# Kernel optimization log

Hardware: AMD Instinct MI355X
Metric: run time of the kernel (lower is better)

The kernel has to match this reference:

```python
import jax, jax.numpy as jnp
import numpy as np
from jax import lax

N, DIM, K, B = 400000, 128, 27, 8


def setup_inputs() -> dict:
    key = jax.random.key(0)
    ks = jax.random.split(key, 8)
    feats = jax.random.normal(ks[0], (N, DIM), dtype=jnp.float32)
    neighbor_idx = jax.random.randint(ks[1], (N, K), 0, N, dtype=jnp.int32)
    neighbor_mask = jax.random.randint(ks[2], (N, K), 0, 2) > 0
    segment_ids = jnp.sort(jax.random.randint(ks[3], (N,), 0, B, dtype=jnp.int32))
    s = 1.0 / np.sqrt(DIM)
    W1 = jax.random.normal(ks[4], (K, DIM, DIM), dtype=jnp.float32) * s
    W2 = jax.random.normal(ks[5], (K, DIM, DIM), dtype=jnp.float32) * s
    W3 = jax.random.normal(ks[6], (DIM, DIM), dtype=jnp.float32) * s
    b1 = jnp.zeros((DIM,), jnp.float32)
    b2 = jnp.zeros((DIM,), jnp.float32)
    b3 = jnp.zeros((DIM,), jnp.float32)
    return {"feats": feats, "neighbor_idx": neighbor_idx, "neighbor_mask": neighbor_mask,
            "segment_ids": segment_ids, "num_segments": B,
            "W1": W1, "b1": b1, "W2": W2, "b2": b2, "W3": W3, "b3": b3}


def sparse_conv3(x, idx, mask, W, b):
    # x: [N,D]; idx/mask: [N,K]; W: [K,D,D] -> y[n] = sum_k mask[n,k] * x[idx[n,k]] @ W[k] + b
    def step(acc, kin):
        ik, mk, Wk = kin  # [N], [N], [D,D]
        g = jnp.where(mk[:, None], x[ik], 0.0)  # [N,D] gather per offset
        return acc + g @ Wk, None
    acc, _ = lax.scan(step, jnp.zeros_like(x), (idx.T, mask.T, W))
    return acc + b


def reference(feats, neighbor_idx, neighbor_mask, segment_ids, num_segments,
              W1, b1, W2, b2, W3, b3):
    out1 = jax.nn.relu(sparse_conv3(feats, neighbor_idx, neighbor_mask, W1, b1))
    out2 = jax.nn.relu(sparse_conv3(feats, neighbor_idx, neighbor_mask, W2, b2))
    # per-batch: outer(mean over channels of out1 [Ni,1], mean over points of out2 [1,D])
    sums = jax.ops.segment_sum(out2, segment_ids, num_segments=num_segments)  # [B,D]
    cnts = jax.ops.segment_sum(jnp.ones((out2.shape[0],), out2.dtype), segment_ids,
                               num_segments=num_segments)  # [B]
    seg_mean2 = sums / jnp.maximum(cnts, 1.0)[:, None]  # [B,D]
    row_mean1 = jnp.mean(out1, axis=-1, keepdims=True)  # [N,1]
    enc = jnp.sqrt(row_mean1 * seg_mean2[segment_ids] + 1e-12)  # [N,D]
    mid = enc + out1 + out2
    out3 = jax.nn.relu(mid @ W3 + b3)  # kernel_size=1 conv == pointwise linear
    return jax.nn.relu(feats - out3)
```

## Files before the change

### kernel.cpp

```cpp
#include <hip/hip_runtime.h>
#include <stdint.h>

#define NPTS 400000
#define DIM  128
#define KNB  27
#define NSEG 8

typedef _Float16 f16x8 __attribute__((ext_vector_type(8)));
typedef float floatx16 __attribute__((ext_vector_type(16)));

#define OFF_FEATSH 0UL
#define OFF_OUT1   102400000UL
#define OFF_OUT2   204800000UL
#define OFF_PW1    307200000UL
#define OFF_PW2    308084736UL
#define OFF_PW3    308969472UL
#define OFF_SEG    309002240UL
#define OFF_CNT    309006336UL

__device__ __forceinline__ void load_lds16(const void* g, void* l) {
  __builtin_amdgcn_global_load_lds(
      (const __attribute__((address_space(1))) void*)g,
      (__attribute__((address_space(3))) void*)l, 16, 0, 0);
}

__global__ __launch_bounds__(256) void cvt_feats(const float* __restrict__ f,
                                                 _Float16* __restrict__ fh) {
  size_t g = (size_t)blockIdx.x * 256 + threadIdx.x;
  const float4* src = (const float4*)f;
  float4 v0 = src[g * 2], v1 = src[g * 2 + 1];
  f16x8 o;
  o[0] = (_Float16)v0.x; o[1] = (_Float16)v0.y; o[2] = (_Float16)v0.z; o[3] = (_Float16)v0.w;
  o[4] = (_Float16)v1.x; o[5] = (_Float16)v1.y; o[6] = (_Float16)v1.z; o[7] = (_Float16)v1.w;
  ((f16x8*)fh)[g] = o;
}

__global__ __launch_bounds__(256) void pack_w(const float* __restrict__ W1,
                                              const float* __restrict__ W2,
                                              const float* __restrict__ W3,
                                              _Float16* __restrict__ pW1,
                                              _Float16* __restrict__ pW2,
                                              _Float16* __restrict__ pW3) {
  int gid = blockIdx.x * 256 + threadIdx.x;
  const float* W; _Float16* dst; int k, rem;
  if (gid < 110592) {
    int mat = gid / 55296, r = gid % 55296;
    W = mat ? W2 : W1; dst = (mat ? pW2 : pW1) + (size_t)r * 8;
    k = r >> 11; rem = r & 2047;
  } else {
    int r = gid - 110592;
    W = W3; dst = pW3 + (size_t)r * 8; k = 0; rem = r;
  }
  int ko = rem >> 8, ct = (rem >> 6) & 3, lane = rem & 63;
  int h = lane >> 5, c = ct * 32 + (lane & 31);
  f16x8 o;
#pragma unroll
  for (int j = 0; j < 8; ++j) {
    int kk = ko * 16 + h * 8 + j;
    o[j] = (_Float16)W[(size_t)(k * 128 + kk) * 128 + c];
  }
  *(f16x8*)dst = o;
}

__global__ __launch_bounds__(256, 2) void conv_kernel(
    const _Float16* __restrict__ featsh, const int* __restrict__ nidx,
    const int* __restrict__ nmask, const int* __restrict__ segids,
    const _Float16* __restrict__ pW1, const _Float16* __restrict__ pW2,
    const float* __restrict__ b1, const float* __restrict__ b2,
    _Float16* __restrict__ out1, _Float16* __restrict__ out2,
    float* __restrict__ seg_sums, float* __restrict__ cnts_f) {
  __shared__ __align__(16) char lds_raw[65536];
  int tid = threadIdx.x, w = tid >> 6, lane = tid & 63;
  int conv = w >> 1, g = w & 1, h = lane >> 5;
  int n0 = blockIdx.x * 128;
  int row0 = n0 + g * 64 + (lane & 31);
  int row1 = row0 + 32;

  floatx16 acc0[4], acc1[4];
#pragma unroll
  for (int ct = 0; ct < 4; ++ct)
#pragma unroll
    for (int r = 0; r < 16; ++r) { acc0[ct][r] = 0.f; acc1[ct][r] = 0.f; }

  const char* srcW = (const char*)(w < 2 ? pW1 : pW2) + (w & 1) * 16384;

  for (int k = 0; k < KNB; ++k) {
    __syncthreads();
    const char* sk = srcW + (size_t)k * 32768;
    char* ldsb = lds_raw + w * 16384;
#pragma unroll
    for (int it = 0; it < 16; ++it)
      load_lds16(sk + it * 1024 + lane * 16, ldsb + it * 1024);
    int i0 = nidx[row0 * KNB + k]; int m0 = nmask[row0 * KNB + k];
    int i1 = nidx[row1 * KNB + k]; int m1 = nmask[row1 * KNB + k];
    __syncthreads();
    const _Float16* ldsW = (const _Float16*)(lds_raw + conv * 32768);
    const _Float16* ar0 = featsh + (size_t)i0 * 128 + h * 8;
    const _Float16* ar1 = featsh + (size_t)i1 * 128 + h * 8;
#pragma unroll
    for (int ko = 0; ko < 8; ++ko) {
      uint4 a0u = {0, 0, 0, 0}, a1u = {0, 0, 0, 0};
      if (m0) a0u = *(const uint4*)(ar0 + ko * 16);
      if (m1) a1u = *(const uint4*)(ar1 + ko * 16);
      f16x8 a0 = __builtin_bit_cast(f16x8, a0u);
      f16x8 a1 = __builtin_bit_cast(f16x8, a1u);
#pragma unroll
      for (int ct = 0; ct < 4; ++ct) {
        f16x8 b = *(const f16x8*)(ldsW + ((ko * 4 + ct) * 64 + lane) * 8);
        acc0[ct] = __builtin_amdgcn_mfma_f32_32x32x16_f16(a0, b, acc0[ct], 0, 0, 0);
        acc1[ct] = __builtin_amdgcn_mfma_f32_32x32x16_f16(a1, b, acc1[ct], 0, 0, 0);
      }
    }
  }

  const float* bb = conv ? b2 : b1;
  float bias[4];
#pragma unroll
  for (int ct = 0; ct < 4; ++ct) bias[ct] = bb[ct * 32 + (lane & 31)];
#pragma unroll
  for (int ct = 0; ct < 4; ++ct)
#pragma unroll
    for (int r = 0; r < 16; ++r) {
      acc0[ct][r] = fmaxf(acc0[ct][r] + bias[ct], 0.f);
      acc1[ct][r] = fmaxf(acc1[ct][r] + bias[ct], 0.f);
    }

  int seg0 = segids[n0];
  bool uniform = (seg0 == segids[n0 + 127]);

  if (conv == 1 && uniform) {
#pragma unroll
    for (int ct = 0; ct < 4; ++ct) {
      float s = 0.f;
#pragma unroll
      for (int r = 0; r < 16; ++r) s += acc0[ct][r] + acc1[ct][r];
      s += __shfl_xor(s, 32);
      if (lane < 32) atomicAdd(&seg_sums[seg0 * 128 + ct * 32 + lane], s);
    }
  }
  if (tid == 0 && uniform) atomicAdd(&cnts_f[seg0], 128.0f);

  __syncthreads();
  _Float16* lds_out = (_Float16*)lds_raw;
#pragma unroll
  for (int ct = 0; ct < 4; ++ct) {
    int col = ct * 32 + (lane & 31);
#pragma unroll
    for (int r = 0; r < 16; ++r) {
      int lr = g * 64 + (r & 3) + 8 * (r >> 2) + 4 * h;
      lds_out[conv * 16384 + lr * 128 + col] = (_Float16)acc0[ct][r];
      lds_out[conv * 16384 + (lr + 32) * 128 + col] = (_Float16)acc1[ct][r];
    }
  }
  __syncthreads();

  if (!uniform && tid < 128) {
    int s = segids[n0 + tid];
    atomicAdd(&cnts_f[s], 1.0f);
    for (int c = 0; c < 128; ++c)
      atomicAdd(&seg_sums[s * 128 + c], (float)lds_out[16384 + tid * 128 + c]);
  }

#pragma unroll
  for (int it = 0; it < 16; ++it) {
    int chunk = it * 256 + tid;
    int cv = chunk >> 11;
    int off16 = chunk & 2047;
    uint4 v = *(const uint4*)(lds_raw + cv * 32768 + off16 * 16);
    *(uint4*)((cv ? out2 : out1) + (size_t)n0 * 128 + off16 * 8) = v;
  }
}

__global__ __launch_bounds__(256, 2) void final_kernel(
    const float* __restrict__ feats, const _Float16* __restrict__ out1,
    const _Float16* __restrict__ out2, const int* __restrict__ segids,
    const float* __restrict__ seg_sums, const float* __restrict__ cnts_f,
    const char* __restrict__ pW3, const float* __restrict__ b3,
    float* __restrict__ dout) {
  __shared__ __align__(16) char ldsw3[32768];
  __shared__ float smean[NSEG * 128];
  int tid = threadIdx.x, w = tid >> 6, lane = tid & 63, h = lane >> 5;
  int n0 = blockIdx.x * 128;
#pragma unroll
  for (int it = 0; it < 8; ++it)
    load_lds16(pW3 + w * 8192 + it * 1024 + lane * 16, ldsw3 + w * 8192 + it * 1024);
  for (int i = tid; i < NSEG * 128; i += 256)
    smean[i] = seg_sums[i] / fmaxf(cnts_f[i >> 7], 1.0f);
  __syncthreads();

  int row = n0 + w * 32 + (lane & 31);
  int seg = segids[row];
  const char* p1 = (const char*)(out1 + (size_t)row * 128 + h * 8);
  const char* p2 = (const char*)(out2 + (size_t)row * 128 + h * 8);
  f16x8 o1[8], o2[8];
  float s1 = 0.f;
#pragma unroll
  for (int ko = 0; ko < 8; ++ko) {
    o1[ko] = *(const f16x8*)(p1 + ko * 32);
    o2[ko] = *(const f16x8*)(p2 + ko * 32);
#pragma unroll
    for (int j = 0; j < 8; ++j) s1 += (float)o1[ko][j];
  }
  s1 += __shfl_xor(s1, 32);
  float rm = s1 * (1.0f / 128.0f);

  f16x8 a[8];
#pragma unroll
  for (int ko = 0; ko < 8; ++ko) {
    int colb = ko * 16 + h * 8;
#pragma unroll
    for (int j = 0; j < 8; ++j) {
      float m2 = smean[seg * 128 + colb + j];
      float e = sqrtf(fmaf(rm, m2, 1e-12f));
      a[ko][j] = (_Float16)(e + (float)o1[ko][j] + (float)o2[ko][j]);
    }
  }
  floatx16 acc[4];
#pragma unroll
  for (int ct = 0; ct < 4; ++ct)
#pragma unroll
    for (int r = 0; r < 16; ++r) acc[ct][r] = 0.f;
#pragma unroll
  for (int ko = 0; ko < 8; ++ko)
#pragma unroll
    for (int ct = 0; ct < 4; ++ct) {
      f16x8 b = *(const f16x8*)(ldsw3 + ((ko * 4 + ct) * 64 + lane) * 16);
      acc[ct] = __builtin_amdgcn_mfma_f32_32x32x16_f16(a[ko], b, acc[ct], 0, 0, 0);
    }
#pragma unroll
  for (int ct = 0; ct < 4; ++ct) {
    int col = ct * 32 + (lane & 31);
    float bc = b3[col];
#pragma unroll
    for (int r = 0; r < 16; ++r) {
      int gr = n0 + w * 32 + (r & 3) + 8 * (r >> 2) + 4 * h;
      float v = fmaxf(acc[ct][r] + bc, 0.f);
      float f = feats[(size_t)gr * 128 + col];
      dout[(size_t)gr * 128 + col] = fmaxf(f - v, 0.f);
    }
  }
}

extern "C" void kernel_launch(void* const* d_in, const int* in_sizes, int n_in,
                              void* d_out, int out_size, void* d_ws, size_t ws_size,
                              hipStream_t stream) {
  (void)in_sizes; (void)n_in; (void)out_size; (void)ws_size;
  const float* feats = (const float*)d_in[0];
  const int* nidx   = (const int*)d_in[1];
  const int* nmask  = (const int*)d_in[2];
  const int* segids = (const int*)d_in[3];
  const float* W1 = (const float*)d_in[5];
  const float* b1 = (const float*)d_in[6];
  const float* W2 = (const float*)d_in[7];
  const float* b2 = (const float*)d_in[8];
  const float* W3 = (const float*)d_in[9];
  const float* b3 = (const float*)d_in[10];
  float* dout = (float*)d_out;
  char* ws = (char*)d_ws;

  _Float16* featsh = (_Float16*)(ws + OFF_FEATSH);
  _Float16* out1h  = (_Float16*)(ws + OFF_OUT1);
  _Float16* out2h  = (_Float16*)(ws + OFF_OUT2);
  _Float16* pW1    = (_Float16*)(ws + OFF_PW1);
  _Float16* pW2    = (_Float16*)(ws + OFF_PW2);
  _Float16* pW3    = (_Float16*)(ws + OFF_PW3);
  float* seg_sums  = (float*)(ws + OFF_SEG);
  float* cnts_f    = (float*)(ws + OFF_CNT);

  hipMemsetAsync(ws + OFF_SEG, 0, 4096 + 32, stream);
  cvt_feats<<<25000, 256, 0, stream>>>(feats, featsh);
  pack_w<<<440, 256, 0, stream>>>(W1, W2, W3, pW1, pW2, pW3);
  conv_kernel<<<3125, 256, 0, stream>>>(featsh, nidx, nmask, segids, pW1, pW2,
                                        b1, b2, out1h, out2h, seg_sums, cnts_f);
  final_kernel<<<3125, 256, 0, stream>>>(feats, out1h, out2h, segids, seg_sums,
                                         cnts_f, (const char*)pW3, b3, dout);
}
```

Before: 1.670 ms.

## Read weights directly from global memory, stage neighbor indices in LDS, batch gathers

```diff
diff --git a/kernel.cpp b/kernel.cpp
--- a/kernel.cpp
+++ b/kernel.cpp
@@ -73,8 +73,19 @@
   int tid = threadIdx.x, w = tid >> 6, lane = tid & 63;
   int conv = w >> 1, g = w & 1, h = lane >> 5;
   int n0 = blockIdx.x * 128;
-  int row0 = n0 + g * 64 + (lane & 31);
-  int row1 = row0 + 32;
+  int rl0 = g * 64 + (lane & 31);
+  int rl1 = rl0 + 32;
+
+  int* lds_idx = (int*)lds_raw;
+  int* lds_msk = (int*)(lds_raw + 13824);
+  {
+    const uint4* gi = (const uint4*)(nidx + (size_t)n0 * KNB);
+    const uint4* gm = (const uint4*)(nmask + (size_t)n0 * KNB);
+    uint4* di = (uint4*)lds_idx;
+    uint4* dm = (uint4*)lds_msk;
+    for (int c = tid; c < 864; c += 256) { di[c] = gi[c]; dm[c] = gm[c]; }
+  }
+  __syncthreads();
 
   floatx16 acc0[4], acc1[4];
 #pragma unroll
@@ -82,31 +93,27 @@
 #pragma unroll
     for (int r = 0; r < 16; ++r) { acc0[ct][r] = 0.f; acc1[ct][r] = 0.f; }
 
-  const char* srcW = (const char*)(w < 2 ? pW1 : pW2) + (w & 1) * 16384;
+  const char* pB = (const char*)(conv ? pW2 : pW1) + (size_t)lane * 16;
 
   for (int k = 0; k < KNB; ++k) {
-    __syncthreads();
-    const char* sk = srcW + (size_t)k * 32768;
-    char* ldsb = lds_raw + w * 16384;
-#pragma unroll
-    for (int it = 0; it < 16; ++it)
-      load_lds16(sk + it * 1024 + lane * 16, ldsb + it * 1024);
-    int i0 = nidx[row0 * KNB + k]; int m0 = nmask[row0 * KNB + k];
-    int i1 = nidx[row1 * KNB + k]; int m1 = nmask[row1 * KNB + k];
-    __syncthreads();
-    const _Float16* ldsW = (const _Float16*)(lds_raw + conv * 32768);
+    int i0 = lds_idx[rl0 * KNB + k], m0 = lds_msk[rl0 * KNB + k];
+    int i1 = lds_idx[rl1 * KNB + k], m1 = lds_msk[rl1 * KNB + k];
     const _Float16* ar0 = featsh + (size_t)i0 * 128 + h * 8;
     const _Float16* ar1 = featsh + (size_t)i1 * 128 + h * 8;
+    uint4 a0u[8], a1u[8];
 #pragma unroll
     for (int ko = 0; ko < 8; ++ko) {
-      uint4 a0u = {0, 0, 0, 0}, a1u = {0, 0, 0, 0};
-      if (m0) a0u = *(const uint4*)(ar0 + ko * 16);
-      if (m1) a1u = *(const uint4*)(ar1 + ko * 16);
-      f16x8 a0 = __builtin_bit_cast(f16x8, a0u);
-      f16x8 a1 = __builtin_bit_cast(f16x8, a1u);
+      uint4 z = {0, 0, 0, 0};
+      a0u[ko] = m0 ? *(const uint4*)(ar0 + ko * 16) : z;
+      a1u[ko] = m1 ? *(const uint4*)(ar1 + ko * 16) : z;
+    }
+#pragma unroll
+    for (int ko = 0; ko < 8; ++ko) {
+      f16x8 a0 = __builtin_bit_cast(f16x8, a0u[ko]);
+      f16x8 a1 = __builtin_bit_cast(f16x8, a1u[ko]);
 #pragma unroll
       for (int ct = 0; ct < 4; ++ct) {
-        f16x8 b = *(const f16x8*)(ldsW + ((ko * 4 + ct) * 64 + lane) * 8);
+        f16x8 b = *(const f16x8*)(pB + (size_t)((k * 8 + ko) * 4 + ct) * 1024);
         acc0[ct] = __builtin_amdgcn_mfma_f32_32x32x16_f16(a0, b, acc0[ct], 0, 0, 0);
         acc1[ct] = __builtin_amdgcn_mfma_f32_32x32x16_f16(a1, b, acc1[ct], 0, 0, 0);
       }
```

Result: slower. 2.550 ms (+52.7%).
